# Optimization experiments

Measured on AMD Instinct MI355X. Metric: run time of the kernel, lower is better.

The kernel has to match this reference:

```python
import jax, jax.numpy as jnp
import numpy as np

FM = 32          # feature_maps
OUT_BITS = 16    # output_bits
PASS_STEPS = 3
N_EDGES = 3_200_000
VAR_COUNT = 100_000
CONST_COUNT = 50_000
EPS = 1e-5       # torch LayerNorm default


def _ln(x):
    # LayerNorm over last dim, elementwise_affine=False
    mu = jnp.mean(x, axis=-1, keepdims=True)
    var = jnp.mean((x - mu) ** 2, axis=-1, keepdims=True)
    return (x - mu) / jnp.sqrt(var + EPS)


def _mlp_ln(x, W1, b1, W2, b2):
    # Linear -> ReLU -> Linear -> LayerNorm(no affine)
    return _ln(jax.nn.relu(x @ W1 + b1) @ W2 + b2)


def _linear_init(key, fan_in, fan_out):
    kW, kb = jax.random.split(key)
    bound = 1.0 / np.sqrt(fan_in)
    W = jax.random.uniform(kW, (fan_in, fan_out), jnp.float32, -bound, bound)
    b = jax.random.uniform(kb, (fan_out,), jnp.float32, -bound, bound)
    return W, b


def setup_inputs() -> dict:
    key = jax.random.key(0)
    ks = jax.random.split(key, 12)
    inp = {}
    inp["edge_var"] = jax.random.randint(ks[0], (N_EDGES,), 0, VAR_COUNT, dtype=jnp.int64 if jax.config.jax_enable_x64 else jnp.int32)
    inp["edge_const"] = jax.random.randint(ks[1], (N_EDGES,), 0, CONST_COUNT, dtype=jnp.int64 if jax.config.jax_enable_x64 else jnp.int32)
    inp["edge_val"] = jax.random.normal(ks[2], (N_EDGES,), jnp.float32)
    inp["conditions_values"] = jax.random.normal(ks[3], (CONST_COUNT,), jnp.float32)
    inp["var_count"] = VAR_COUNT
    inp["const_count"] = CONST_COUNT
    # prepare_cond: 1 -> 2*fm -> fm
    inp["pc_W1"], inp["pc_b1"] = _linear_init(ks[4], 1, 2 * FM)
    inp["pc_W2"], inp["pc_b2"] = _linear_init(ks[5], 2 * FM, FM)
    # constraint_update: 3*fm -> 2*fm -> fm
    inp["cu_W1"], inp["cu_b1"] = _linear_init(ks[6], 3 * FM, 2 * FM)
    inp["cu_W2"], inp["cu_b2"] = _linear_init(ks[7], 2 * FM, FM)
    # variable_update: 2*fm -> 2*fm -> fm
    inp["vu_W1"], inp["vu_b1"] = _linear_init(ks[8], 2 * FM, 2 * FM)
    inp["vu_W2"], inp["vu_b2"] = _linear_init(ks[9], 2 * FM, FM)
    # output: fm -> 2*fm -> output_bits
    inp["out_W1"], inp["out_b1"] = _linear_init(ks[10], FM, 2 * FM)
    inp["out_W2"], inp["out_b2"] = _linear_init(ks[11], 2 * FM, OUT_BITS)
    return inp


def reference(edge_var, edge_const, edge_val, conditions_values, var_count, const_count,
              pc_W1, pc_b1, pc_W2, pc_b2,
              cu_W1, cu_b1, cu_W2, cu_b2,
              vu_W1, vu_b1, vu_W2, vu_b2,
              out_W1, out_b1, out_W2, out_b2):
    variables = jnp.ones((var_count, FM), dtype=edge_val.dtype)
    emb = _mlp_ln(conditions_values[:, None], pc_W1, pc_b1, pc_W2, pc_b2)  # [C, fm]
    constraints = emb
    ev = edge_val[:, None]
    for _ in range(PASS_STEPS):
        # adj.T @ variables : scatter-add variable features into constraints
        v2c = jax.ops.segment_sum(variables[edge_var] * ev, edge_const, num_segments=const_count)
        constraints = _mlp_ln(jnp.concatenate([constraints, emb, v2c], axis=-1),
                              cu_W1, cu_b1, cu_W2, cu_b2)
        # adj @ constraints : scatter-add constraint features into variables
        c2v = jax.ops.segment_sum(constraints[edge_const] * ev, edge_var, num_segments=var_count)
        variables = _mlp_ln(jnp.concatenate([variables, c2v], axis=-1),
                            vu_W1, vu_b1, vu_W2, vu_b2)
    out = jax.nn.relu(variables @ out_W1 + out_b1) @ out_W2 + out_b2
    return jax.nn.sigmoid(out)
```

## Files before the change

kernel.cpp:

```cpp
#include <hip/hip_runtime.h>
#include <hip/hip_fp16.h>
#include <math.h>

#define FM 32
#define N_EDGES 3200000
#define VAR_COUNT 100000
#define CONST_COUNT 50000
#define LN_EPS 1e-5f

#define EPB 4096
#define ABLK 782
#define HABLK 391
#define NB 782
#define AB2 784
#define LSTRIDE 784

typedef _Float16 f16;
typedef __attribute__((ext_vector_type(4))) _Float16 f16x4;
typedef __attribute__((ext_vector_type(4))) float f32x4;

static __device__ __forceinline__ float warp_sum32(float v) {
#pragma unroll
    for (int m = 16; m; m >>= 1) v += __shfl_xor(v, m);
    return v;
}

__global__ void init_vars(float* __restrict__ v, __half* __restrict__ v16, int n) {
    int i = blockIdx.x * 256 + threadIdx.x;
    if (i < n) {
        if (v) v[i] = 1.0f;
        if (v16) v16[i] = __float2half(1.0f);
    }
}


template <int DSHIFT>
__global__ __launch_bounds__(256) void bucket_sort(
    const int* __restrict__ dest_arr, const int* __restrict__ src_arr,
    const float* __restrict__ val_arr,
    int2* __restrict__ recs_tmp, int* __restrict__ lscan, int* __restrict__ rlen_T,
    int n) {
    __shared__ int hist[NB];
    __shared__ int cursor[NB];
    __shared__ int chunk[256];
    __shared__ int2 stage[EPB];
    const int t = threadIdx.x;
    const int base = blockIdx.x * EPB;
    const int nb = min(EPB, n - base);
    for (int i = t; i < NB; i += 256) hist[i] = 0;
    __syncthreads();
    int dg[16], pk[16], vb[16];
#pragma unroll
    for (int k = 0; k < 16; ++k) {
        int j = k * 256 + t;
        dg[k] = -1;
        if (j < nb) {
            int dest = dest_arr[base + j];
            int src  = src_arr[base + j];
            vb[k] = __float_as_int(val_arr[base + j]);
            dg[k] = dest >> DSHIFT;
            pk[k] = ((dest & ((1 << DSHIFT) - 1)) << 20) | src;
            atomicAdd(&hist[dg[k]], 1);
        }
    }
    __syncthreads();
    int sum = 0;
#pragma unroll
    for (int k = 0; k < 4; ++k) {
        int idx = t * 4 + k;
        if (idx < NB) sum += hist[idx];
    }
    chunk[t] = sum;
    __syncthreads();
    for (int off = 1; off < 256; off <<= 1) {
        int v = (t >= off) ? chunk[t - off] : 0;
        __syncthreads();
        chunk[t] += v;
        __syncthreads();
    }
    int run = chunk[t] - sum;
#pragma unroll
    for (int k = 0; k < 4; ++k) {
        int idx = t * 4 + k;
        if (idx < NB) {
            int h = hist[idx];
            rlen_T[(size_t)idx * AB2 + blockIdx.x] = h;
            hist[idx] = run;
            cursor[idx] = run;
            run += h;
        }
    }
    __syncthreads();
    {
        int* lp = lscan + (size_t)blockIdx.x * LSTRIDE;
        for (int i = t; i < NB; i += 256) lp[i] = hist[i];
        if (t == 0) lp[NB] = nb;
    }
#pragma unroll
    for (int k = 0; k < 16; ++k) {
        if (dg[k] >= 0) {
            int pos = atomicAdd(&cursor[dg[k]], 1);
            stage[pos] = make_int2(pk[k], vb[k]);
        }
    }
    __syncthreads();
    for (int j = t; j < nb; j += 256) recs_tmp[(size_t)base + j] = stage[j];
}

__global__ __launch_bounds__(256) void row_sum(const int* __restrict__ rlen_T,
                                               int* __restrict__ btot) {
    __shared__ int ls[256];
    const int t = threadIdx.x;
    const int blk = blockIdx.x;
    const int h = (blk >= NB) ? 1 : 0;
    const int k = blk - h * NB;
    const int* rp = rlen_T + (size_t)k * AB2 + h * HABLK;
    int s = 0;
    for (int b = t; b < HABLK; b += 256) s += rp[b];
    ls[t] = s;
    __syncthreads();
    for (int off = 128; off; off >>= 1) {
        if (t < off) ls[t] += ls[t + off];
        __syncthreads();
    }
    if (t == 0) btot[blk] = ls[0];
}

__global__ __launch_bounds__(256) void scan_btot(
    const int* __restrict__ btot, int* __restrict__ bb, int n, int total) {
    __shared__ int ls[256];
    const int t = threadIdx.x;
    int a[8];
    const int idx = t * 8;
    int tsum = 0;
#pragma unroll
    for (int u = 0; u < 8; ++u) {
        a[u] = (idx + u < n) ? btot[idx + u] : 0;
        tsum += a[u];
    }
    ls[t] = tsum;
    __syncthreads();
    for (int off = 1; off < 256; off <<= 1) {
        int v = (t >= off) ? ls[t - off] : 0;
        __syncthreads();
        ls[t] += v;
        __syncthreads();
    }
    int excl = ls[t] - tsum;
#pragma unroll
    for (int u = 0; u < 8; ++u) {
        if (idx + u < n) bb[idx + u] = excl;
        excl += a[u];
    }
    if (t == 0) bb[n] = total;
}


template <int DSHIFT, int NDEST>
__global__ __launch_bounds__(256) void collect_sort(
    const int2* __restrict__ recs_tmp, const int* __restrict__ lscan,
    const int* __restrict__ rlen_T, const int* __restrict__ bb,
    int2* __restrict__ recs_out, int* __restrict__ offs0, int* __restrict__ offs1,
    float* __restrict__ wsum0, float* __restrict__ wsum1, int nrows) {
    __shared__ int hist[NDEST];
    __shared__ int cursor[NDEST];
    __shared__ int sc[NDEST];
    __shared__ float wsumL[NDEST];
    const int t = threadIdx.x;
    const int blk = blockIdx.x;
    const int h = (blk >= NB) ? 1 : 0;
    const int k = blk - h * NB;
    const int bsb = h * HABLK;
    int* __restrict__ offsH = h ? offs1 : offs0;
    float* __restrict__ wsumH = (wsum0 == nullptr) ? nullptr : (h ? wsum1 : wsum0);
    const int c0 = t * 2, c1 = t * 2 + 1;
    int s0 = 0, l0 = 0, s1 = 0, l1 = 0;
    if (c0 < HABLK) { s0 = lscan[(size_t)(bsb + c0) * LSTRIDE + k]; l0 = rlen_T[(size_t)k * AB2 + bsb + c0]; }
    if (c1 < HABLK) { s1 = lscan[(size_t)(bsb + c1) * LSTRIDE + k]; l1 = rlen_T[(size_t)k * AB2 + bsb + c1]; }
    const int2* rp0 = recs_tmp + (size_t)(bsb + c0) * EPB + s0;
    const int2* rp1 = recs_tmp + (size_t)(bsb + c1) * EPB + s1;
    for (int i = t; i < NDEST; i += 256) { hist[i] = 0; wsumL[i] = 0.0f; }
    __syncthreads();
    for (int j = 0; j < l0; ++j) {
        int2 r = rp0[j];
        atomicAdd(&hist[r.x >> 20], 1);
        if (wsumH) atomicAdd(&wsumL[r.x >> 20], __int_as_float(r.y));
    }
    for (int j = 0; j < l1; ++j) {
        int2 r = rp1[j];
        atomicAdd(&hist[r.x >> 20], 1);
        if (wsumH) atomicAdd(&wsumL[r.x >> 20], __int_as_float(r.y));
    }
    __syncthreads();
    if (t < NDEST) sc[t] = hist[t];
    __syncthreads();
    for (int off = 1; off < NDEST; off <<= 1) {
        int v = (t >= off && t < NDEST) ? sc[t - off] : 0;
        __syncthreads();
        if (t < NDEST) sc[t] += v;
        __syncthreads();
    }
    if (t < NDEST) {
        int excl = sc[t] - hist[t];
        cursor[t] = excl;
        int gd = (k << DSHIFT) + t;
        if (gd <= nrows) offsH[gd] = bb[blk] + excl;
        if (wsumH && gd < nrows) wsumH[gd] = wsumL[t];
    }
    __syncthreads();
    const int base_out = bb[blk];
    for (int j = 0; j < l0; ++j) {
        int2 r = rp0[j];
        int pos = atomicAdd(&cursor[r.x >> 20], 1);
        recs_out[(size_t)base_out + pos] = make_int2(r.x & 0xFFFFF, r.y);
    }
    for (int j = 0; j < l1; ++j) {
        int2 r = rp1[j];
        int pos = atomicAdd(&cursor[r.x >> 20], 1);
        recs_out[(size_t)base_out + pos] = make_int2(r.x & 0xFFFFF, r.y);
    }
}


__global__ __launch_bounds__(256) void seg_gather16(
    const int* __restrict__ offs0, const int* __restrict__ offs1,
    const int2* __restrict__ recs,
    const __half* __restrict__ src16, __half* __restrict__ dst16, int nrows) {
    const int g = threadIdx.x >> 4, f2 = threadIdx.x & 15;
    const int row = blockIdx.x * 16 + g;
    if (row >= nrows) return;
    const __half2* __restrict__ s2 = (const __half2*)src16;
    float ax[8], ay[8];
#pragma unroll
    for (int u = 0; u < 8; ++u) { ax[u] = 0.0f; ay[u] = 0.0f; }
    for (int h = 0; h < 2; ++h) {
        const int* __restrict__ of = h ? offs1 : offs0;
        int j = of[row];
        const int j1 = of[row + 1];
        for (; j + 8 <= j1; j += 8) {
            int2 r[8];
#pragma unroll
            for (int u = 0; u < 8; ++u) r[u] = recs[j + u];
            __half2 hh[8];
#pragma unroll
            for (int u = 0; u < 8; ++u) hh[u] = s2[(size_t)r[u].x * 16 + f2];
#pragma unroll
            for (int u = 0; u < 8; ++u) {
                float w = __int_as_float(r[u].y);
                float2 f = __half22float2(hh[u]);
                ax[u] = fmaf(f.x, w, ax[u]);
                ay[u] = fmaf(f.y, w, ay[u]);
            }
        }
        for (; j < j1; ++j) {
            int2 ra = recs[j];
            __half2 ha = s2[(size_t)ra.x * 16 + f2];
            float wa = __int_as_float(ra.y);
            float2 fa = __half22float2(ha);
            ax[0] = fmaf(fa.x, wa, ax[0]);
            ay[0] = fmaf(fa.y, wa, ay[0]);
        }
    }
    float rx = ((ax[0] + ax[1]) + (ax[2] + ax[3])) + ((ax[4] + ax[5]) + (ax[6] + ax[7]));
    float ry = ((ay[0] + ay[1]) + (ay[2] + ay[3])) + ((ay[4] + ay[5]) + (ay[6] + ay[7]));
    ((__half2*)dst16)[(size_t)row * 16 + f2] = __floats2half2_rn(rx, ry);
}


__global__ __launch_bounds__(256) void scatter_edges(
    const int* __restrict__ src_idx, const int* __restrict__ dst_idx,
    const float* __restrict__ ev, const float* __restrict__ src,
    float* __restrict__ dst, int n_edges) {
    int e = blockIdx.x * 8 + (threadIdx.x >> 5);
    int f = threadIdx.x & 31;
    if (e >= n_edges) return;
    atomicAdd(&dst[(size_t)dst_idx[e] * FM + f], src[(size_t)src_idx[e] * FM + f] * ev[e]);
}


template <int NSEG>
__global__ __launch_bounds__(256) void mlp_mfma(
    const __half* __restrict__ s0h, const __half* __restrict__ s1h,
    const __half* __restrict__ s2h,
    const float* __restrict__ ws0, const float* __restrict__ ws1,
    const float* __restrict__ W1, const float* __restrict__ b1,
    const float* __restrict__ W2, const float* __restrict__ b2,
    __half* __restrict__ dst16, int nrows) {
    constexpr int KT = NSEG * 2;
    __shared__ float hbuf[4][16][68];
    const int t = threadIdx.x;
    const int w = t >> 6;
    const int L = t & 63;
    const int c = L & 15;
    const int g = L >> 4;
    f16x4 B1[KT * 4];
#pragma unroll
    for (int kt = 0; kt < KT; ++kt) {
#pragma unroll
        for (int jt = 0; jt < 4; ++jt) {
            f16x4 bf;
#pragma unroll
            for (int i = 0; i < 4; ++i)
                bf[i] = (f16)W1[(size_t)(kt * 16 + 4 * g + i) * 64 + jt * 16 + c];
            B1[kt * 4 + jt] = bf;
        }
    }
    f16x4 B2[8];
#pragma unroll
    for (int kt = 0; kt < 4; ++kt) {
#pragma unroll
        for (int ct = 0; ct < 2; ++ct) {
            f16x4 bf;
#pragma unroll
            for (int i = 0; i < 4; ++i)
                bf[i] = (f16)W2[(size_t)(kt * 16 + 4 * g + i) * 32 + ct * 16 + c];
            B2[kt * 2 + ct] = bf;
        }
    }
    float b1v[4];
#pragma unroll
    for (int jt = 0; jt < 4; ++jt) b1v[jt] = b1[jt * 16 + c];
    const float b2v0 = b2[c], b2v1 = b2[16 + c];
    const f16* sa0 = (const f16*)s0h;
    const f16* sa1 = (const f16*)s1h;
    const f16* sa2 = (const f16*)s2h;

    const int step = gridDim.x * 4 * 16;
    for (int r0 = (blockIdx.x * 4 + w) * 16; r0 < nrows; r0 += step) {
        const int arow = r0 + c;
        f32x4 C1[4];
#pragma unroll
        for (int jt = 0; jt < 4; ++jt) {
            C1[jt][0] = 0.0f; C1[jt][1] = 0.0f; C1[jt][2] = 0.0f; C1[jt][3] = 0.0f;
        }
        f16x4 wsfrag;
        if (NSEG == 3 && ws0) {
            f16 wv = (f16)(ws0[arow] + ws1[arow]);
            wsfrag[0] = wv; wsfrag[1] = wv; wsfrag[2] = wv; wsfrag[3] = wv;
        }
#pragma unroll
        for (int kt = 0; kt < KT; ++kt) {
            f16x4 a;
            if (NSEG == 3 && kt >= 4 && ws0) {
                a = wsfrag;
            } else {
                const f16* sp = (kt < 2) ? sa0 : ((kt < 4) ? sa1 : sa2);
                a = *(const f16x4*)(sp + (size_t)arow * FM + (kt & 1) * 16 + 4 * g);
            }
#pragma unroll
            for (int jt = 0; jt < 4; ++jt)
                C1[jt] = __builtin_amdgcn_mfma_f32_16x16x16f16(a, B1[kt * 4 + jt],
                                                               C1[jt], 0, 0, 0);
        }
#pragma unroll
        for (int jt = 0; jt < 4; ++jt)
#pragma unroll
            for (int j = 0; j < 4; ++j)
                hbuf[w][4 * g + j][jt * 16 + c] = fmaxf(C1[jt][j] + b1v[jt], 0.0f);
        asm volatile("s_waitcnt lgkmcnt(0)" ::: "memory");
        f16x4 A2[4];
#pragma unroll
        for (int kt = 0; kt < 4; ++kt) {
            float4 hv = *(const float4*)&hbuf[w][c][kt * 16 + 4 * g];
            f16x4 af;
            af[0] = (f16)hv.x; af[1] = (f16)hv.y; af[2] = (f16)hv.z; af[3] = (f16)hv.w;
            A2[kt] = af;
        }
        f32x4 C2[2];
        C2[0][0] = 0.0f; C2[0][1] = 0.0f; C2[0][2] = 0.0f; C2[0][3] = 0.0f;
        C2[1][0] = 0.0f; C2[1][1] = 0.0f; C2[1][2] = 0.0f; C2[1][3] = 0.0f;
#pragma unroll
        for (int kt = 0; kt < 4; ++kt) {
            C2[0] = __builtin_amdgcn_mfma_f32_16x16x16f16(A2[kt], B2[kt * 2 + 0],
                                                          C2[0], 0, 0, 0);
            C2[1] = __builtin_amdgcn_mfma_f32_16x16x16f16(A2[kt], B2[kt * 2 + 1],
                                                          C2[1], 0, 0, 0);
        }
#pragma unroll
        for (int j = 0; j < 4; ++j) {
            float y0 = C2[0][j] + b2v0;
            float y1 = C2[1][j] + b2v1;
            float s = y0 + y1;
            s += __shfl_xor(s, 1); s += __shfl_xor(s, 2);
            s += __shfl_xor(s, 4); s += __shfl_xor(s, 8);
            float mu = s * (1.0f / 32.0f);
            float d0 = y0 - mu, d1 = y1 - mu;
            float q = d0 * d0 + d1 * d1;
            q += __shfl_xor(q, 1); q += __shfl_xor(q, 2);
            q += __shfl_xor(q, 4); q += __shfl_xor(q, 8);
            float rs = rsqrtf(q * (1.0f / 32.0f) + LN_EPS);
            const size_t rbase = (size_t)(r0 + 4 * g + j) * FM;
            dst16[rbase + c]      = __float2half(d0 * rs);
            dst16[rbase + 16 + c] = __float2half(d1 * rs);
        }
    }
}


__global__ __launch_bounds__(256) void pc_mlp(
    const float* __restrict__ cond,
    const float* __restrict__ W1, const float* __restrict__ b1,
    const float* __restrict__ W2, const float* __restrict__ b2,
    float* __restrict__ dstA, float* __restrict__ dstB,
    __half* __restrict__ dstA16, __half* __restrict__ dstB16, int nrows) {
    __shared__ float sW2[64 * FM];
    __shared__ float sh[4][64];
    for (int i = threadIdx.x; i < 64 * FM; i += 256) sW2[i] = W2[i];
    int g = threadIdx.x >> 6, l = threadIdx.x & 63, l32 = l & 31, half = l >> 5;
    float w1l = W1[l], b1l = b1[l], b2l = b2[l32];
    __syncthreads();
    for (int row = blockIdx.x * 4 + g; row < nrows; row += gridDim.x * 4) {
        float cc = cond[row];
        sh[g][l] = fmaxf(fmaf(cc, w1l, b1l), 0.0f);
        float y = 0.0f;
#pragma unroll
        for (int k = 0; k < 32; k += 4) {
            float4 hv = *(const float4*)&sh[g][half * 32 + k];
            y = fmaf(hv.x, sW2[(half * 32 + k + 0) * FM + l32], y);
            y = fmaf(hv.y, sW2[(half * 32 + k + 1) * FM + l32], y);
            y = fmaf(hv.z, sW2[(half * 32 + k + 2) * FM + l32], y);
            y = fmaf(hv.w, sW2[(half * 32 + k + 3) * FM + l32], y);
        }
        y += __shfl_xor(y, 32);
        y += b2l;
        float s = warp_sum32(y);
        float mu = s * (1.0f / 32.0f);
        float d = y - mu;
        float v = warp_sum32(d * d);
        if (half == 0) {
            float o = d * rsqrtf(v * (1.0f / 32.0f) + LN_EPS);
            if (dstA)   dstA[(size_t)row * FM + l32] = o;
            if (dstB)   dstB[(size_t)row * FM + l32] = o;
            if (dstA16) dstA16[(size_t)row * FM + l32] = __float2half(o);
            if (dstB16) dstB16[(size_t)row * FM + l32] = __float2half(o);
        }
    }
}

template <int NSEG>
__global__ __launch_bounds__(256) void mlp_ln_f32(
    const float* __restrict__ s0, const float* __restrict__ s1,
    const float* __restrict__ s2,
    const float* __restrict__ W1, const float* __restrict__ b1,
    const float* __restrict__ W2, const float* __restrict__ b2,
    float* __restrict__ dst, __half* __restrict__ dst16, int nrows) {
    constexpr int IN = NSEG * FM;
    __shared__ float sW2[64 * FM];
    __shared__ float sx[4][IN];
    __shared__ float sh[4][64];
    for (int i = threadIdx.x; i < 64 * FM; i += 256) sW2[i] = W2[i];
    int g = threadIdx.x >> 6, l = threadIdx.x & 63, l32 = l & 31, half = l >> 5;
    float w1r[IN];
#pragma unroll
    for (int k = 0; k < IN; ++k) w1r[k] = W1[k * 64 + l];
    float b1l = b1[l], b2l = b2[l32];
    __syncthreads();
    for (int row = blockIdx.x * 4 + g; row < nrows; row += gridDim.x * 4) {
#pragma unroll
        for (int i = l; i < IN; i += 64) {
            const float* s = (i < 32) ? s0 : (i < 64) ? s1 : s2;
            sx[g][i] = s[(size_t)row * FM + (i & 31)];
        }
        float acc = b1l;
#pragma unroll
        for (int k = 0; k < IN; k += 4) {
            float4 xv = *(const float4*)&sx[g][k];
            acc = fmaf(xv.x, w1r[k + 0], acc);
            acc = fmaf(xv.y, w1r[k + 1], acc);
            acc = fmaf(xv.z, w1r[k + 2], acc);
            acc = fmaf(xv.w, w1r[k + 3], acc);
        }
        sh[g][l] = fmaxf(acc, 0.0f);
        float y = 0.0f;
#pragma unroll
        for (int k = 0; k < 32; k += 4) {
            float4 hv = *(const float4*)&sh[g][half * 32 + k];
            y = fmaf(hv.x, sW2[(half * 32 + k + 0) * FM + l32], y);
            y = fmaf(hv.y, sW2[(half * 32 + k + 1) * FM + l32], y);
            y = fmaf(hv.z, sW2[(half * 32 + k + 2) * FM + l32], y);
            y = fmaf(hv.w, sW2[(half * 32 + k + 3) * FM + l32], y);
        }
        y += __shfl_xor(y, 32);
        y += b2l;
        float s = warp_sum32(y);
        float mu = s * (1.0f / 32.0f);
        float d = y - mu;
        float v = warp_sum32(d * d);
        if (half == 0) {
            float o = d * rsqrtf(v * (1.0f / 32.0f) + LN_EPS);
            dst[(size_t)row * FM + l32] = o;
            if (dst16) dst16[(size_t)row * FM + l32] = __float2half(o);
        }
    }
}

__global__ __launch_bounds__(256) void out_mlp(
    const __half* __restrict__ x16,
    const float* __restrict__ W1, const float* __restrict__ b1,
    const float* __restrict__ W2, const float* __restrict__ b2,
    float* __restrict__ dst, int nrows) {
    __shared__ float sW2[64 * 16];
    __shared__ float sx[4][FM];
    __shared__ float sh[4][64];
    for (int i = threadIdx.x; i < 64 * 16; i += 256) sW2[i] = W2[i];
    int g = threadIdx.x >> 6, l = threadIdx.x & 63;
    int o = l & 15, q = l >> 4;
    float w1r[FM];
#pragma unroll
    for (int k = 0; k < FM; ++k) w1r[k] = W1[k * 64 + l];
    float b1l = b1[l];
    float b2o = b2[o];
    __syncthreads();
    for (int row = blockIdx.x * 4 + g; row < nrows; row += gridDim.x * 4) {
        if (l < FM) sx[g][l] = __half2float(x16[(size_t)row * FM + l]);
        float acc = b1l;
#pragma unroll
        for (int k = 0; k < FM; k += 4) {
            float4 xv = *(const float4*)&sx[g][k];
            acc = fmaf(xv.x, w1r[k + 0], acc);
            acc = fmaf(xv.y, w1r[k + 1], acc);
            acc = fmaf(xv.z, w1r[k + 2], acc);
            acc = fmaf(xv.w, w1r[k + 3], acc);
        }
        sh[g][l] = fmaxf(acc, 0.0f);
        float y = 0.0f;
#pragma unroll
        for (int k = 0; k < 16; k += 4) {
            int kk = q * 16 + k;
            float4 hv = *(const float4*)&sh[g][kk];
            y = fmaf(hv.x, sW2[(kk + 0) * 16 + o], y);
            y = fmaf(hv.y, sW2[(kk + 1) * 16 + o], y);
            y = fmaf(hv.z, sW2[(kk + 2) * 16 + o], y);
            y = fmaf(hv.w, sW2[(kk + 3) * 16 + o], y);
        }
        y += __shfl_xor(y, 16);
        y += __shfl_xor(y, 32);
        if (q == 0) dst[(size_t)row * 16 + o] = 1.0f / (1.0f + expf(-(y + b2o)));
    }
}


extern "C" void kernel_launch(void* const* d_in, const int* in_sizes, int n_in,
                              void* d_out, int out_size, void* d_ws, size_t ws_size,
                              hipStream_t stream) {
    const int*   edge_var   = (const int*)d_in[0];
    const int*   edge_const = (const int*)d_in[1];
    const float* edge_val   = (const float*)d_in[2];
    const float* cond       = (const float*)d_in[3];
    const float* pc_W1 = (const float*)d_in[6];
    const float* pc_b1 = (const float*)d_in[7];
    const float* pc_W2 = (const float*)d_in[8];
    const float* pc_b2 = (const float*)d_in[9];
    const float* cu_W1 = (const float*)d_in[10];
    const float* cu_b1 = (const float*)d_in[11];
    const float* cu_W2 = (const float*)d_in[12];
    const float* cu_b2 = (const float*)d_in[13];
    const float* vu_W1 = (const float*)d_in[14];
    const float* vu_b1 = (const float*)d_in[15];
    const float* vu_W2 = (const float*)d_in[16];
    const float* vu_b2 = (const float*)d_in[17];
    const float* out_W1 = (const float*)d_in[18];
    const float* out_b1 = (const float*)d_in[19];
    const float* out_W2 = (const float*)d_in[20];
    const float* out_b2 = (const float*)d_in[21];

    float* ws = (float*)d_ws;
    size_t off = 0;
    auto alloc = [&](size_t nelems) {
        float* p = ws + off;
        off += (nelems + 15) & ~(size_t)15;
        return p;
    };
    __half* vars16  = (__half*)alloc(VAR_COUNT * FM / 2);
    __half* cons16  = (__half*)alloc(CONST_COUNT * FM / 2);
    __half* emb16   = (__half*)alloc(CONST_COUNT * FM / 2);
    __half* msg16   = (__half*)alloc(VAR_COUNT * FM / 2);
    int2*   recs_t  = (int2*)alloc((size_t)N_EDGES * 2);
    int2*   recs_c  = (int2*)alloc((size_t)N_EDGES * 2);
    int2*   recs_v  = (int2*)alloc((size_t)N_EDGES * 2);
    int*    lscan   = (int*)alloc((size_t)ABLK * LSTRIDE);
    int*    rlen_T  = (int*)alloc((size_t)NB * AB2);
    int*    btot    = (int*)alloc(2 * NB);
    int*    bb_c    = (int*)alloc(2 * NB + 1);
    int*    bb_v    = (int*)alloc(2 * NB + 1);
    int*    offs_c0 = (int*)alloc(CONST_COUNT + 1);
    int*    offs_c1 = (int*)alloc(CONST_COUNT + 1);
    int*    offs_v0 = (int*)alloc(VAR_COUNT + 1);
    int*    offs_v1 = (int*)alloc(VAR_COUNT + 1);
    float*  wsum_c0 = alloc(CONST_COUNT);
    float*  wsum_c1 = alloc(CONST_COUNT);
    size_t need_bytes = off * sizeof(float);
    bool fast = ws_size >= need_bytes;

    float* emb  = (float*)recs_t;
    float* cons = emb + CONST_COUNT * FM;
    float* vars = cons + CONST_COUNT * FM;
    float* msg  = (float*)recs_c;

    if (fast) {
        bucket_sort<6><<<ABLK, 256, 0, stream>>>(edge_const, edge_var, edge_val,
                                                 recs_t, lscan, rlen_T, N_EDGES);
        row_sum<<<2 * NB, 256, 0, stream>>>(rlen_T, btot);
        scan_btot<<<1, 256, 0, stream>>>(btot, bb_c, 2 * NB, N_EDGES);
        collect_sort<6, 64><<<2 * NB, 256, 0, stream>>>(
            recs_t, lscan, rlen_T, bb_c, recs_c, offs_c0, offs_c1,
            wsum_c0, wsum_c1, CONST_COUNT);
        bucket_sort<7><<<ABLK, 256, 0, stream>>>(edge_var, edge_const, edge_val,
                                                 recs_t, lscan, rlen_T, N_EDGES);
        row_sum<<<2 * NB, 256, 0, stream>>>(rlen_T, btot);
        scan_btot<<<1, 256, 0, stream>>>(btot, bb_v, 2 * NB, N_EDGES);
        collect_sort<7, 128><<<2 * NB, 256, 0, stream>>>(
            recs_t, lscan, rlen_T, bb_v, recs_v, offs_v0, offs_v1,
            nullptr, nullptr, VAR_COUNT);

        init_vars<<<(VAR_COUNT * FM + 255) / 256, 256, 0, stream>>>(
            nullptr, vars16, VAR_COUNT * FM);
        pc_mlp<<<1024, 256, 0, stream>>>(cond, pc_W1, pc_b1, pc_W2, pc_b2,
                                         nullptr, nullptr, emb16, cons16, CONST_COUNT);

        for (int pass = 0; pass < 3; ++pass) {
            if (pass == 0) {
                mlp_mfma<3><<<512, 256, 0, stream>>>(
                    cons16, emb16, nullptr, wsum_c0, wsum_c1,
                    cu_W1, cu_b1, cu_W2, cu_b2, cons16, CONST_COUNT);
            } else {
                seg_gather16<<<(CONST_COUNT + 15) / 16, 256, 0, stream>>>(
                    offs_c0, offs_c1, recs_c, vars16, msg16, CONST_COUNT);
                mlp_mfma<3><<<512, 256, 0, stream>>>(
                    cons16, emb16, msg16, nullptr, nullptr,
                    cu_W1, cu_b1, cu_W2, cu_b2, cons16, CONST_COUNT);
            }
            seg_gather16<<<(VAR_COUNT + 15) / 16, 256, 0, stream>>>(
                offs_v0, offs_v1, recs_v, cons16, msg16, VAR_COUNT);
            mlp_mfma<2><<<512, 256, 0, stream>>>(
                vars16, msg16, nullptr, nullptr, nullptr,
                vu_W1, vu_b1, vu_W2, vu_b2, vars16, VAR_COUNT);
        }
    } else {
        init_vars<<<(VAR_COUNT * FM + 255) / 256, 256, 0, stream>>>(
            vars, vars16, VAR_COUNT * FM);
        pc_mlp<<<1024, 256, 0, stream>>>(cond, pc_W1, pc_b1, pc_W2, pc_b2,
                                         emb, cons, nullptr, nullptr, CONST_COUNT);
        for (int pass = 0; pass < 3; ++pass) {
            hipMemsetAsync(msg, 0, (size_t)CONST_COUNT * FM * sizeof(float), stream);
            scatter_edges<<<N_EDGES / 8, 256, 0, stream>>>(edge_var, edge_const, edge_val,
                                                           vars, msg, N_EDGES);
            mlp_ln_f32<3><<<1024, 256, 0, stream>>>(cons, emb, msg,
                                                    cu_W1, cu_b1, cu_W2, cu_b2,
                                                    cons, nullptr, CONST_COUNT);
            hipMemsetAsync(msg, 0, (size_t)VAR_COUNT * FM * sizeof(float), stream);
            scatter_edges<<<N_EDGES / 8, 256, 0, stream>>>(edge_const, edge_var, edge_val,
                                                           cons, msg, N_EDGES);
            mlp_ln_f32<2><<<1024, 256, 0, stream>>>(vars, msg, nullptr,
                                                    vu_W1, vu_b1, vu_W2, vu_b2,
                                                    vars, vars16, VAR_COUNT);
        }
    }

    out_mlp<<<1024, 256, 0, stream>>>(vars16, out_W1, out_b1, out_W2, out_b2,
                                      (float*)d_out, VAR_COUNT);
}
```

Baseline: 505.3 us.

## Stage bucket records in LDS for collect_sort and enlarge MLP grids

```diff
diff --git a/kernel.cpp b/kernel.cpp
--- a/kernel.cpp
+++ b/kernel.cpp
@@ -14,6 +14,7 @@
 #define NB 782
 #define AB2 784
 #define LSTRIDE 784
+#define CAPH 2560
 
 typedef _Float16 f16;
 typedef __attribute__((ext_vector_type(4))) _Float16 f16x4;
@@ -162,10 +163,13 @@
     const int* __restrict__ rlen_T, const int* __restrict__ bb,
     int2* __restrict__ recs_out, int* __restrict__ offs0, int* __restrict__ offs1,
     float* __restrict__ wsum0, float* __restrict__ wsum1, int nrows) {
+    __shared__ int2 stage[CAPH];
+    __shared__ int rloff[256];
     __shared__ int hist[NDEST];
     __shared__ int cursor[NDEST];
     __shared__ int sc[NDEST];
     __shared__ float wsumL[NDEST];
+    __shared__ int nb_s;
     const int t = threadIdx.x;
     const int blk = blockIdx.x;
     const int h = (blk >= NB) ? 1 : 0;
@@ -177,17 +181,30 @@
     int s0 = 0, l0 = 0, s1 = 0, l1 = 0;
     if (c0 < HABLK) { s0 = lscan[(size_t)(bsb + c0) * LSTRIDE + k]; l0 = rlen_T[(size_t)k * AB2 + bsb + c0]; }
     if (c1 < HABLK) { s1 = lscan[(size_t)(bsb + c1) * LSTRIDE + k]; l1 = rlen_T[(size_t)k * AB2 + bsb + c1]; }
-    const int2* rp0 = recs_tmp + (size_t)(bsb + c0) * EPB + s0;
-    const int2* rp1 = recs_tmp + (size_t)(bsb + c1) * EPB + s1;
+    int tsum = l0 + l1;
+    rloff[t] = tsum;
+    __syncthreads();
+    for (int off = 1; off < 256; off <<= 1) {
+        int v = (t >= off) ? rloff[t - off] : 0;
+        __syncthreads();
+        rloff[t] += v;
+        __syncthreads();
+    }
+    if (t == 255) nb_s = rloff[255];
+    int o0 = rloff[t] - tsum;
+    int o1 = o0 + l0;
     for (int i = t; i < NDEST; i += 256) { hist[i] = 0; wsumL[i] = 0.0f; }
     __syncthreads();
-    for (int j = 0; j < l0; ++j) {
-        int2 r = rp0[j];
-        atomicAdd(&hist[r.x >> 20], 1);
-        if (wsumH) atomicAdd(&wsumL[r.x >> 20], __int_as_float(r.y));
-    }
-    for (int j = 0; j < l1; ++j) {
-        int2 r = rp1[j];
+    const int nb = min(nb_s, CAPH);
+    {
+        const int2* rp = recs_tmp + (size_t)(bsb + c0) * EPB + s0;
+        for (int j = 0; j < l0; ++j) if (o0 + j < CAPH) stage[o0 + j] = rp[j];
+        rp = recs_tmp + (size_t)(bsb + c1) * EPB + s1;
+        for (int j = 0; j < l1; ++j) if (o1 + j < CAPH) stage[o1 + j] = rp[j];
+    }
+    __syncthreads();
+    for (int j = t; j < nb; j += 256) {
+        int2 r = stage[j];
         atomicAdd(&hist[r.x >> 20], 1);
         if (wsumH) atomicAdd(&wsumL[r.x >> 20], __int_as_float(r.y));
     }
@@ -209,13 +226,8 @@
     }
     __syncthreads();
     const int base_out = bb[blk];
-    for (int j = 0; j < l0; ++j) {
-        int2 r = rp0[j];
-        int pos = atomicAdd(&cursor[r.x >> 20], 1);
-        recs_out[(size_t)base_out + pos] = make_int2(r.x & 0xFFFFF, r.y);
-    }
-    for (int j = 0; j < l1; ++j) {
-        int2 r = rp1[j];
+    for (int j = t; j < nb; j += 256) {
+        int2 r = stage[j];
         int pos = atomicAdd(&cursor[r.x >> 20], 1);
         recs_out[(size_t)base_out + pos] = make_int2(r.x & 0xFFFFF, r.y);
     }
@@ -620,19 +632,19 @@
 
         for (int pass = 0; pass < 3; ++pass) {
             if (pass == 0) {
-                mlp_mfma<3><<<512, 256, 0, stream>>>(
+                mlp_mfma<3><<<782, 256, 0, stream>>>(
                     cons16, emb16, nullptr, wsum_c0, wsum_c1,
                     cu_W1, cu_b1, cu_W2, cu_b2, cons16, CONST_COUNT);
             } else {
                 seg_gather16<<<(CONST_COUNT + 15) / 16, 256, 0, stream>>>(
                     offs_c0, offs_c1, recs_c, vars16, msg16, CONST_COUNT);
-                mlp_mfma<3><<<512, 256, 0, stream>>>(
+                mlp_mfma<3><<<782, 256, 0, stream>>>(
                     cons16, emb16, msg16, nullptr, nullptr,
                     cu_W1, cu_b1, cu_W2, cu_b2, cons16, CONST_COUNT);
             }
             seg_gather16<<<(VAR_COUNT + 15) / 16, 256, 0, stream>>>(
                 offs_v0, offs_v1, recs_v, cons16, msg16, VAR_COUNT);
-            mlp_mfma<2><<<512, 256, 0, stream>>>(
+            mlp_mfma<2><<<1563, 256, 0, stream>>>(
                 vars16, msg16, nullptr, nullptr, nullptr,
                 vu_W1, vu_b1, vu_W2, vu_b2, vars16, VAR_COUNT);
         }
```

Result: faster. 489.1 us (-3.2%).
